# Optimization experiments

Hardware: AMD Instinct MI355X
Metric: run time of the kernel (lower is better)

Reference implementation:

```python
import jax, jax.numpy as jnp
import numpy as np

DIM = 512
CODEBOOK_SIZE = 8192
B, N = 8, 2048
EPS = 1e-12


def setup_inputs() -> dict:
    key = jax.random.key(0)
    k1, k2, k3 = jax.random.split(key, 3)
    x = jax.random.normal(k1, (B, N, DIM), dtype=jnp.float32)
    # matches torch.randn(codebook_size, dim) * dim ** -0.5
    codebook = jax.random.normal(k2, (CODEBOOK_SIZE, DIM), dtype=jnp.float32) * DIM ** -0.5
    # nn.Linear(dim, dim, bias=False) weight, applied as x @ W.T
    W = jax.random.normal(k3, (DIM, DIM), dtype=jnp.float32) * DIM ** -0.5
    return {"x": x, "codebook": codebook, "W": W}


def _l2norm(t):
    return t / jnp.maximum(jnp.linalg.norm(t, axis=-1, keepdims=True), EPS)


def _rotate_from_to(q, x):
    """Rotation trick: forward value == q, gradient flows through x via a
    detached Householder-style rotation (R = I - 2ww^T + 2 q_hat x_hat^T)
    and detached norm rescaling."""
    sg = jax.lax.stop_gradient
    norm_x = jnp.linalg.norm(x, axis=-1, keepdims=True)
    norm_q = jnp.linalg.norm(q, axis=-1, keepdims=True)
    x_hat = x / jnp.maximum(norm_x, EPS)
    q_hat = q / jnp.maximum(norm_q, EPS)
    w = sg(_l2norm(x_hat + q_hat))
    x_hat_d, q_hat_d = sg(x_hat), sg(q_hat)
    e = x
    rotated = (e
               - 2.0 * jnp.sum(e * w, axis=-1, keepdims=True) * w
               + 2.0 * jnp.sum(e * x_hat_d, axis=-1, keepdims=True) * q_hat_d)
    return rotated * sg(norm_q / jnp.maximum(norm_x, EPS))


def reference(x, codebook, W):
    # implicit codebook = Linear(codebook)
    codes = jnp.einsum('cd,ed->ce', codebook, W)  # [C, d]
    d2 = -2.0 * jnp.einsum('bnd,cd->bnc', x, codes) + jnp.sum(codes * codes, axis=-1)
    indices = jnp.argmin(jax.lax.stop_gradient(d2), axis=-1)  # [b, n] int
    quantized = codes[indices]  # gather -> [b, n, d]
    commit_loss = jnp.mean((jax.lax.stop_gradient(x) - quantized) ** 2)
    quantized = _rotate_from_to(quantized, x)
    return quantized, indices, commit_loss
```

## Files before the change

### kernel.cpp

```cpp
#include <hip/hip_runtime.h>


#define DIMK  512
#define CBN   8192
#define MROWS 16384

#define SX 24.0f
#define SC 500.0f
#define INV_SS (1.0f / (SX * SC))
#define DKEY  1231
#define NSLOT 3

#define WS_CODES   0UL
#define WS_XQ      16777216UL
#define WS_CQ      25165824UL
#define WS_NORMS   29360128UL
#define WS_CAND    29392896UL
#define WS_CBH     29392896UL
#define WS_CBL     37781504UL
#define WS_WH      54558720UL
#define WS_WL      55083008UL
#define WS_LOSSP   55607296UL

typedef short s16x8 __attribute__((ext_vector_type(8)));
typedef int   i32x4 __attribute__((ext_vector_type(4)));
typedef float f32x4 __attribute__((ext_vector_type(4)));

__device__ __forceinline__ unsigned short f2bf(float f) {
    unsigned u = __float_as_uint(f);
    unsigned r = u + 0x7FFFu + ((u >> 16) & 1u);
    return (unsigned short)(r >> 16);
}
__device__ __forceinline__ float bf2f(unsigned short h) {
    return __uint_as_float(((unsigned)h) << 16);
}
__device__ __forceinline__ void load_lds16(const void* g, void* l) {
    __builtin_amdgcn_global_load_lds((const __attribute__((address_space(1))) void*)g,
                                     (__attribute__((address_space(3))) void*)l,
                                     16, 0, 0);
}
__device__ __forceinline__ signed char q8(float v, float s) {
    return (signed char)__float2int_rn(fminf(fmaxf(v * s, -127.0f), 127.0f));
}

__global__ __launch_bounds__(256) void prep(
        const float* __restrict__ x, const float* __restrict__ cb, const float* __restrict__ W,
        signed char* __restrict__ xq,
        unsigned short* __restrict__ cbh, unsigned short* __restrict__ cbl,
        unsigned short* __restrict__ wh, unsigned short* __restrict__ wl,
        float* __restrict__ norms) {
    const int b = blockIdx.x;
    const int t = threadIdx.x;
    if (b < 8192) {
        const int i = b * 256 + t;
        float4 v = ((const float4*)x)[i];
        char4 c;
        c.x = q8(v.x, SX); c.y = q8(v.y, SX); c.z = q8(v.z, SX); c.w = q8(v.w, SX);
        ((char4*)xq)[i] = c;
    } else if (b < 12288) {
        const int i = (b - 8192) * 256 + t;
        float4 v = ((const float4*)cb)[i];
        ushort4 h, l;
        h.x = f2bf(v.x); l.x = f2bf(v.x - bf2f(h.x));
        h.y = f2bf(v.y); l.y = f2bf(v.y - bf2f(h.y));
        h.z = f2bf(v.z); l.z = f2bf(v.z - bf2f(h.z));
        h.w = f2bf(v.w); l.w = f2bf(v.w - bf2f(h.w));
        ((ushort4*)cbh)[i] = h;
        ((ushort4*)cbl)[i] = l;
    } else if (b < 12544) {
        const int i = (b - 12288) * 256 + t;
        float4 v = ((const float4*)W)[i];
        ushort4 h, l;
        h.x = f2bf(v.x); l.x = f2bf(v.x - bf2f(h.x));
        h.y = f2bf(v.y); l.y = f2bf(v.y - bf2f(h.y));
        h.z = f2bf(v.z); l.z = f2bf(v.z - bf2f(h.z));
        h.w = f2bf(v.w); l.w = f2bf(v.w - bf2f(h.w));
        ((ushort4*)wh)[i] = h;
        ((ushort4*)wl)[i] = l;
    } else {
        const int i = (b - 12544) * 256 + t;
        norms[i] = 0.0f;
    }
}

__global__ __launch_bounds__(512) void codes_mfma(
        const unsigned short* __restrict__ Ah_g, const unsigned short* __restrict__ Al_g,
        const unsigned short* __restrict__ Bh_g, const unsigned short* __restrict__ Bl_g,
        float* __restrict__ C, signed char* __restrict__ Cq, float* __restrict__ Norms) {
    __shared__ __align__(16) unsigned short Ahi[2][128 * 32];
    __shared__ __align__(16) unsigned short Alo[2][128 * 32];
    __shared__ __align__(16) unsigned short Bhi[2][128 * 32];
    __shared__ __align__(16) unsigned short Blo[2][128 * 32];

    const int t    = threadIdx.x;
    const int w    = t >> 6;
    const int lane = t & 63;
    const int quad = lane >> 4;
    const int l16  = lane & 15;
    const int wm   = w & 3, wn = w >> 2;
    const int rowBase = blockIdx.x * 128;
    const int colBase = blockIdx.y * 128;

    f32x4 acc[2][4];
    #pragma unroll
    for (int i = 0; i < 2; ++i)
        #pragma unroll
        for (int j = 0; j < 4; ++j)
            acc[i][j] = (f32x4)(0.0f);

    const int mr = t >> 2;
    const int kq = ((t & 3) ^ ((t >> 3) & 3)) * 8;
    const size_t gxa = (size_t)(rowBase + mr) * DIMK + kq;
    const size_t gca = (size_t)(colBase + mr) * DIMK + kq;
    const int l0 = w * 512;

    const int swz8 = (quad ^ ((l16 >> 1) & 3)) * 8;

#define CODES_STAGE(NXT, K0)                                   \
    do {                                                       \
        load_lds16(Ah_g + gxa + (K0), &Ahi[NXT][l0]);          \
        load_lds16(Al_g + gxa + (K0), &Alo[NXT][l0]);          \
        load_lds16(Bh_g + gca + (K0), &Bhi[NXT][l0]);          \
        load_lds16(Bl_g + gca + (K0), &Blo[NXT][l0]);          \
    } while (0)

#define CODES_COMPUTE(CUR)                                                                         \
    do {                                                                                           \
        s16x8 ah[2], al[2], bh[4], bl[4];                                                          \
        _Pragma("unroll")                                                                          \
        for (int i = 0; i < 2; ++i) {                                                              \
            const int m = wm * 32 + i * 16 + l16;                                                  \
            ah[i] = *(const s16x8*)&Ahi[CUR][m * 32 + swz8];                                       \
            al[i] = *(const s16x8*)&Alo[CUR][m * 32 + swz8];                                       \
        }                                                                                          \
        _Pragma("unroll")                                                                          \
        for (int j = 0; j < 4; ++j) {                                                              \
            const int n = wn * 64 + j * 16 + l16;                                                  \
            bh[j] = *(const s16x8*)&Bhi[CUR][n * 32 + swz8];                                       \
            bl[j] = *(const s16x8*)&Blo[CUR][n * 32 + swz8];                                       \
        }                                                                                          \
        _Pragma("unroll")                                                                          \
        for (int i = 0; i < 2; ++i)                                                                \
            _Pragma("unroll")                                                                      \
            for (int j = 0; j < 4; ++j) {                                                          \
                acc[i][j] = __builtin_amdgcn_mfma_f32_16x16x32_bf16(ah[i], bh[j], acc[i][j], 0, 0, 0); \
                acc[i][j] = __builtin_amdgcn_mfma_f32_16x16x32_bf16(ah[i], bl[j], acc[i][j], 0, 0, 0); \
                acc[i][j] = __builtin_amdgcn_mfma_f32_16x16x32_bf16(al[i], bh[j], acc[i][j], 0, 0, 0); \
            }                                                                                      \
    } while (0)

    CODES_STAGE(0, 0);
    asm volatile("s_waitcnt vmcnt(0)" ::: "memory");
    __syncthreads();

    for (int k0 = 0; k0 < DIMK; k0 += 64) {
        CODES_STAGE(1, k0 + 32);
        CODES_COMPUTE(0);
        asm volatile("s_waitcnt vmcnt(0)" ::: "memory");
        __syncthreads();
        if (k0 + 64 < DIMK) {
            CODES_STAGE(0, k0 + 64);
            CODES_COMPUTE(1);
            asm volatile("s_waitcnt vmcnt(0)" ::: "memory");
            __syncthreads();
        } else {
            CODES_COMPUTE(1);
        }
    }
#undef CODES_STAGE
#undef CODES_COMPUTE

    #pragma unroll
    for (int i = 0; i < 2; ++i) {
        #pragma unroll
        for (int r = 0; r < 4; ++r) {
            const int row = rowBase + wm * 32 + i * 16 + quad * 4 + r;
            float nsum = 0.0f;
            #pragma unroll
            for (int j = 0; j < 4; ++j) {
                const int col = colBase + wn * 64 + j * 16 + l16;
                const float v = acc[i][j][r];
                C[(size_t)row * DIMK + col] = v;
                Cq[(size_t)row * DIMK + col] = q8(v, SC);
                nsum = fmaf(v, v, nsum);
            }
            nsum += __shfl_xor(nsum, 1, 64);
            nsum += __shfl_xor(nsum, 2, 64);
            nsum += __shfl_xor(nsum, 4, 64);
            nsum += __shfl_xor(nsum, 8, 64);
            if (l16 == 0) atomicAdd(&Norms[row], nsum);
        }
    }
}

__global__ __launch_bounds__(512, 6) void d2_argmin_i8(
        const signed char* __restrict__ Xq,
        const signed char* __restrict__ Cq,
        const float* __restrict__ Norms,
        unsigned* __restrict__ Cand) {
    __shared__ __align__(16) signed char Ash[2][128 * 64];
    __shared__ __align__(16) signed char Bsh[2][128 * 64];

    const int t    = threadIdx.x;
    const int w    = t >> 6;
    const int lane = t & 63;
    const int quad = lane >> 4;
    const int l16  = lane & 15;
    const int wm   = w & 3, wn = w >> 2;
    const int rowBase = blockIdx.x * 128;
    const int colBase = blockIdx.y * 128;

    i32x4 acc[2][4];
    #pragma unroll
    for (int i = 0; i < 2; ++i)
        #pragma unroll
        for (int j = 0; j < 4; ++j)
            acc[i][j] = (i32x4)(0);

    const int mr  = t >> 2;
    const int kcs = ((t & 3) ^ ((t >> 3) & 3)) * 16;
    const size_t gxa = (size_t)(rowBase + mr) * DIMK + kcs;
    const size_t gca = (size_t)(colBase + mr) * DIMK + kcs;
    const int lb = w * 1024;

    const int swz  = (quad ^ ((l16 >> 1) & 3)) * 16;
    const int aoff = (wm * 32 + l16) * 64 + swz;
    const int boff = (wn * 64 + l16) * 64 + swz;

    float nq[4];
    #pragma unroll
    for (int j = 0; j < 4; ++j)
        nq[j] = fmaf(Norms[colBase + wn * 64 + j * 16 + l16], 4096.0f, 65536.0f);

#define D2_STEP(CUR, NXT, K0, DO_STAGE, DO_SYNC)                                                   \
    do {                                                                                           \
        if (DO_STAGE) {                                                                            \
            load_lds16(Xq + gxa + (K0) + 64, &Ash[NXT][lb]);                                       \
            load_lds16(Cq + gca + (K0) + 64, &Bsh[NXT][lb]);                                       \
        }                                                                                          \
        i32x4 af0 = *(const i32x4*)&Ash[CUR][aoff];                                                \
        i32x4 af1 = *(const i32x4*)&Ash[CUR][aoff + 1024];                                         \
        _Pragma("unroll")                                                                          \
        for (int j = 0; j < 4; ++j) {                                                              \
            const i32x4 bfj = *(const i32x4*)&Bsh[CUR][boff + j * 1024];                           \
            acc[0][j] = __builtin_amdgcn_mfma_i32_16x16x64_i8(af0, bfj, acc[0][j], 0, 0, 0);       \
            acc[1][j] = __builtin_amdgcn_mfma_i32_16x16x64_i8(af1, bfj, acc[1][j], 0, 0, 0);       \
        }                                                                                          \
        if (DO_SYNC) {                                                                             \
            asm volatile("s_waitcnt vmcnt(0)" ::: "memory");                                       \
            __syncthreads();                                                                       \
        }                                                                                          \
    } while (0)

    load_lds16(Xq + gxa, &Ash[0][lb]);
    load_lds16(Cq + gca, &Bsh[0][lb]);
    asm volatile("s_waitcnt vmcnt(0)" ::: "memory");
    __syncthreads();

    D2_STEP(0, 1,   0, true,  true);
    D2_STEP(1, 0,  64, true,  true);
    D2_STEP(0, 1, 128, true,  true);
    D2_STEP(1, 0, 192, true,  true);
    D2_STEP(0, 1, 256, true,  true);
    D2_STEP(1, 0, 320, true,  true);
    D2_STEP(0, 1, 384, true,  true);
    D2_STEP(1, 0, 448, false, false);
#undef D2_STEP

    const unsigned colG = colBase + wn * 64 + l16;
    const int subtile = blockIdx.y * 2 + wn;
    const float C2 = -8192.0f * INV_SS;

    #pragma unroll
    for (int i = 0; i < 2; ++i) {
        #pragma unroll
        for (int r = 0; r < 4; ++r) {
            unsigned k[4];
            #pragma unroll
            for (int j = 0; j < 4; ++j) {
                const float kf = fmaf((float)acc[i][j][r], C2, nq[j]);
                int ki = (int)kf;
                ki = ki < 0 ? 0 : ki;
                ki = ki > 524287 ? 524287 : ki;
                k[j] = ((unsigned)ki << 13) | (colG + j * 16);
            }
            unsigned lo01 = min(k[0], k[1]), hi01 = max(k[0], k[1]);
            unsigned lo23 = min(k[2], k[3]), hi23 = max(k[2], k[3]);
            unsigned a0 = min(lo01, lo23);
            unsigned m  = max(lo01, lo23);
            unsigned tt = min(hi01, hi23);
            unsigned a1 = min(m, tt);
            unsigned a2 = max(m, tt);
            #pragma unroll
            for (int mk = 1; mk < 16; mk <<= 1) {
                const unsigned b0 = __shfl_xor(a0, mk, 64);
                const unsigned b1 = __shfl_xor(a1, mk, 64);
                const unsigned b2 = __shfl_xor(a2, mk, 64);
                const unsigned M0 = max(a0, b0);
                const unsigned m1 = min(a1, b1);
                const unsigned n0 = min(a0, b0);
                a2 = min(max(m1, M0), min(a2, b2));
                a1 = min(M0, m1);
                a0 = n0;
            }
            if (l16 == 0) {
                const int row = rowBase + wm * 32 + i * 16 + quad * 4 + r;
                unsigned* slot = Cand + ((size_t)row * 128 + subtile) * NSLOT;
                slot[0] = a0; slot[1] = a1; slot[2] = a2;
            }
        }
    }
}

__global__ __launch_bounds__(256) void refine_gather(
        const float* __restrict__ X, const float* __restrict__ Codes,
        const float* __restrict__ Norms, const unsigned* __restrict__ Cand,
        float* __restrict__ outQ, float* __restrict__ outIdx,
        float* __restrict__ lossP) {
    const int t    = threadIdx.x;
    const int w    = t >> 6;
    const int lane = t & 63;
    const int row  = blockIdx.x * 4 + w;

    const unsigned* cp = Cand + (size_t)row * 128 * NSLOT + lane * 6;
    unsigned sl[6];
    #pragma unroll
    for (int s = 0; s < 6; ++s) sl[s] = cp[s];

    unsigned mn = sl[0];
    #pragma unroll
    for (int s = 1; s < 6; ++s) mn = min(mn, sl[s]);
    #pragma unroll
    for (int mask = 1; mask < 64; mask <<= 1)
        mn = min(mn, (unsigned)__shfl((int)mn, lane ^ mask, 64));
    const unsigned thrp = (((mn >> 13) + DKEY) << 13) | 0x1FFFu;

    const float4 xa = *(const float4*)(X + (size_t)row * DIMK + lane * 8);
    const float4 xb = *(const float4*)(X + (size_t)row * DIMK + lane * 8 + 4);

    float bestD = __builtin_inff();
    unsigned bestIdx = 0xFFFFFFFFu;

    #pragma unroll
    for (int s = 0; s < 6; ++s) {
        unsigned long long bm = __ballot(sl[s] <= thrp);
        while (bm) {
            const int src = __ffsll(bm) - 1;
            bm &= bm - 1;
            const unsigned sv = (unsigned)__shfl((int)sl[s], src, 64);
            const unsigned idx = sv & 0x1FFFu;
            const float4 ca = *(const float4*)(Codes + (size_t)idx * DIMK + lane * 8);
            const float4 cbv = *(const float4*)(Codes + (size_t)idx * DIMK + lane * 8 + 4);
            float s2 = xa.x * ca.x + xa.y * ca.y + xa.z * ca.z + xa.w * ca.w
                     + xb.x * cbv.x + xb.y * cbv.y + xb.z * cbv.z + xb.w * cbv.w;
            #pragma unroll
            for (int mm = 1; mm < 64; mm <<= 1) s2 += __shfl_xor(s2, mm, 64);
            const float d2 = fmaf(-2.0f, s2, Norms[idx]);
            if (d2 < bestD || (d2 == bestD && idx < bestIdx)) { bestD = d2; bestIdx = idx; }
        }
    }

    const float4 qa = *(const float4*)(Codes + (size_t)bestIdx * DIMK + lane * 8);
    const float4 qb = *(const float4*)(Codes + (size_t)bestIdx * DIMK + lane * 8 + 4);
    *(float4*)(outQ + (size_t)row * DIMK + lane * 8) = qa;
    *(float4*)(outQ + (size_t)row * DIMK + lane * 8 + 4) = qb;
    float dx0 = xa.x - qa.x, dx1 = xa.y - qa.y, dx2 = xa.z - qa.z, dx3 = xa.w - qa.w;
    float dy0 = xb.x - qb.x, dy1 = xb.y - qb.y, dy2 = xb.z - qb.z, dy3 = xb.w - qb.w;
    float s = dx0 * dx0 + dx1 * dx1 + dx2 * dx2 + dx3 * dx3
            + dy0 * dy0 + dy1 * dy1 + dy2 * dy2 + dy3 * dy3;
    #pragma unroll
    for (int off = 32; off > 0; off >>= 1) s += __shfl_down(s, off);
    if (lane == 0) {
        lossP[row] = s;
        outIdx[row] = (float)bestIdx;
    }
}

__global__ __launch_bounds__(1024) void finalize_loss(const float* __restrict__ lossPartials,
                                                      float* __restrict__ outLoss) {
    const int t = threadIdx.x;
    const float4* p = (const float4*)lossPartials;
    const float4 a = p[t];
    const float4 b = p[t + 1024];
    const float4 c = p[t + 2048];
    const float4 d = p[t + 3072];
    float s = (a.x + a.y + a.z + a.w) + (b.x + b.y + b.z + b.w)
            + (c.x + c.y + c.z + c.w) + (d.x + d.y + d.z + d.w);
    #pragma unroll
    for (int off = 32; off > 0; off >>= 1) s += __shfl_down(s, off);
    __shared__ float red[16];
    if ((t & 63) == 0) red[t >> 6] = s;
    __syncthreads();
    if (t < 64) {
        float v = (t < 16) ? red[t] : 0.0f;
        v += __shfl_down(v, 8, 64);
        v += __shfl_down(v, 4, 64);
        v += __shfl_down(v, 2, 64);
        v += __shfl_down(v, 1, 64);
        if (t == 0)
            *outLoss = v * (1.0f / (float)((size_t)MROWS * DIMK));
    }
}

extern "C" void kernel_launch(void* const* d_in, const int* in_sizes, int n_in,
                              void* d_out, int out_size, void* d_ws, size_t ws_size,
                              hipStream_t stream) {
    const float* x  = (const float*)d_in[0];
    const float* cb = (const float*)d_in[1];
    const float* W  = (const float*)d_in[2];
    float* out = (float*)d_out;

    char* ws = (char*)d_ws;
    float* codes          = (float*)(ws + WS_CODES);
    signed char* xq       = (signed char*)(ws + WS_XQ);
    signed char* cq       = (signed char*)(ws + WS_CQ);
    float* norms          = (float*)(ws + WS_NORMS);
    unsigned* cand        = (unsigned*)(ws + WS_CAND);
    unsigned short* cbh   = (unsigned short*)(ws + WS_CBH);
    unsigned short* cbl   = (unsigned short*)(ws + WS_CBL);
    unsigned short* wh    = (unsigned short*)(ws + WS_WH);
    unsigned short* wl    = (unsigned short*)(ws + WS_WL);
    float* lossP          = (float*)(ws + WS_LOSSP);

    prep<<<12576, 256, 0, stream>>>(x, cb, W, xq, cbh, cbl, wh, wl, norms);

    codes_mfma<<<dim3(CBN / 128, DIMK / 128), 512, 0, stream>>>(cbh, cbl, wh, wl, codes, cq, norms);

    d2_argmin_i8<<<dim3(MROWS / 128, CBN / 128), 512, 0, stream>>>(xq, cq, norms, cand);

    refine_gather<<<MROWS / 4, 256, 0, stream>>>(x, codes, norms, cand, out,
                                                 out + (size_t)MROWS * DIMK, lossP);
    finalize_loss<<<1, 1024, 0, stream>>>(lossP, out + (size_t)MROWS * DIMK + MROWS);
}
```

Baseline: 265.4 us.

## Halve codes GEMM N-tile, raise MFMA priority, skip refine for single candidate

The codes GEMM tile shrinks from 128x128 to 128x64, doubling the grid to 512 blocks so more CUs are busy. Half the waves now load the B hi part and half the lo part. The int8 distance kernel wraps its MFMA burst in s_setprio to favour the matrix issue over the loads. The refine kernel counts candidates first and, when exactly one survives the threshold, takes it directly and skips the fp32 dot-product rescoring. These are unrelated changes to three kernels, and the smaller GEMM tile lowers data reuse per block.

```diff
diff --git a/kernel.cpp b/kernel.cpp
--- a/kernel.cpp
+++ b/kernel.cpp
@@ -89,8 +89,8 @@
         float* __restrict__ C, signed char* __restrict__ Cq, float* __restrict__ Norms) {
     __shared__ __align__(16) unsigned short Ahi[2][128 * 32];
     __shared__ __align__(16) unsigned short Alo[2][128 * 32];
-    __shared__ __align__(16) unsigned short Bhi[2][128 * 32];
-    __shared__ __align__(16) unsigned short Blo[2][128 * 32];
+    __shared__ __align__(16) unsigned short Bhi[2][64 * 32];
+    __shared__ __align__(16) unsigned short Blo[2][64 * 32];
 
     const int t    = threadIdx.x;
     const int w    = t >> 6;
@@ -99,34 +99,36 @@
     const int l16  = lane & 15;
     const int wm   = w & 3, wn = w >> 2;
     const int rowBase = blockIdx.x * 128;
-    const int colBase = blockIdx.y * 128;
-
-    f32x4 acc[2][4];
+    const int colBase = blockIdx.y * 64;
+
+    f32x4 acc[2][2];
     #pragma unroll
     for (int i = 0; i < 2; ++i)
         #pragma unroll
-        for (int j = 0; j < 4; ++j)
+        for (int j = 0; j < 2; ++j)
             acc[i][j] = (f32x4)(0.0f);
 
-    const int mr = t >> 2;
-    const int kq = ((t & 3) ^ ((t >> 3) & 3)) * 8;
-    const size_t gxa = (size_t)(rowBase + mr) * DIMK + kq;
-    const size_t gca = (size_t)(colBase + mr) * DIMK + kq;
-    const int l0 = w * 512;
+    const int kqA = ((t & 3) ^ ((t >> 3) & 3)) * 8;
+    const size_t gxa = (size_t)(rowBase + (t >> 2)) * DIMK + kqA;
+    const int la = w * 512;
+    const int u   = (w & 3) * 64 + lane;
+    const int kqB = ((u & 3) ^ ((u >> 3) & 3)) * 8;
+    const size_t gcb = (size_t)(colBase + (u >> 2)) * DIMK + kqB;
+    const int lb2 = (w & 3) * 512;
 
     const int swz8 = (quad ^ ((l16 >> 1) & 3)) * 8;
 
-#define CODES_STAGE(NXT, K0)                                   \
-    do {                                                       \
-        load_lds16(Ah_g + gxa + (K0), &Ahi[NXT][l0]);          \
-        load_lds16(Al_g + gxa + (K0), &Alo[NXT][l0]);          \
-        load_lds16(Bh_g + gca + (K0), &Bhi[NXT][l0]);          \
-        load_lds16(Bl_g + gca + (K0), &Blo[NXT][l0]);          \
+#define CODES_STAGE(NXT, K0)                                       \
+    do {                                                           \
+        load_lds16(Ah_g + gxa + (K0), &Ahi[NXT][la]);              \
+        load_lds16(Al_g + gxa + (K0), &Alo[NXT][la]);              \
+        if (w < 4) load_lds16(Bh_g + gcb + (K0), &Bhi[NXT][lb2]);  \
+        else       load_lds16(Bl_g + gcb + (K0), &Blo[NXT][lb2]);  \
     } while (0)
 
 #define CODES_COMPUTE(CUR)                                                                         \
     do {                                                                                           \
-        s16x8 ah[2], al[2], bh[4], bl[4];                                                          \
+        s16x8 ah[2], al[2], bh[2], bl[2];                                                          \
         _Pragma("unroll")                                                                          \
         for (int i = 0; i < 2; ++i) {                                                              \
             const int m = wm * 32 + i * 16 + l16;                                                  \
@@ -134,15 +136,15 @@
             al[i] = *(const s16x8*)&Alo[CUR][m * 32 + swz8];                                       \
         }                                                                                          \
         _Pragma("unroll")                                                                          \
-        for (int j = 0; j < 4; ++j) {                                                              \
-            const int n = wn * 64 + j * 16 + l16;                                                  \
+        for (int j = 0; j < 2; ++j) {                                                              \
+            const int n = wn * 32 + j * 16 + l16;                                                  \
             bh[j] = *(const s16x8*)&Bhi[CUR][n * 32 + swz8];                                       \
             bl[j] = *(const s16x8*)&Blo[CUR][n * 32 + swz8];                                       \
         }                                                                                          \
         _Pragma("unroll")                                                                          \
         for (int i = 0; i < 2; ++i)                                                                \
             _Pragma("unroll")                                                                      \
-            for (int j = 0; j < 4; ++j) {                                                          \
+            for (int j = 0; j < 2; ++j) {                                                          \
                 acc[i][j] = __builtin_amdgcn_mfma_f32_16x16x32_bf16(ah[i], bh[j], acc[i][j], 0, 0, 0); \
                 acc[i][j] = __builtin_amdgcn_mfma_f32_16x16x32_bf16(ah[i], bl[j], acc[i][j], 0, 0, 0); \
                 acc[i][j] = __builtin_amdgcn_mfma_f32_16x16x32_bf16(al[i], bh[j], acc[i][j], 0, 0, 0); \
@@ -177,8 +179,8 @@
             const int row = rowBase + wm * 32 + i * 16 + quad * 4 + r;
             float nsum = 0.0f;
             #pragma unroll
-            for (int j = 0; j < 4; ++j) {
-                const int col = colBase + wn * 64 + j * 16 + l16;
+            for (int j = 0; j < 2; ++j) {
+                const int col = colBase + wn * 32 + j * 16 + l16;
                 const float v = acc[i][j][r];
                 C[(size_t)row * DIMK + col] = v;
                 Cq[(size_t)row * DIMK + col] = q8(v, SC);
@@ -240,12 +242,14 @@
         }                                                                                          \
         i32x4 af0 = *(const i32x4*)&Ash[CUR][aoff];                                                \
         i32x4 af1 = *(const i32x4*)&Ash[CUR][aoff + 1024];                                         \
+        __builtin_amdgcn_s_setprio(1);                                                             \
         _Pragma("unroll")                                                                          \
         for (int j = 0; j < 4; ++j) {                                                              \
             const i32x4 bfj = *(const i32x4*)&Bsh[CUR][boff + j * 1024];                           \
             acc[0][j] = __builtin_amdgcn_mfma_i32_16x16x64_i8(af0, bfj, acc[0][j], 0, 0, 0);       \
             acc[1][j] = __builtin_amdgcn_mfma_i32_16x16x64_i8(af1, bfj, acc[1][j], 0, 0, 0);       \
         }                                                                                          \
+        __builtin_amdgcn_s_setprio(0);                                                             \
         if (DO_SYNC) {                                                                             \
             asm volatile("s_waitcnt vmcnt(0)" ::: "memory");                                       \
             __syncthreads();                                                                       \
@@ -335,28 +339,40 @@
         mn = min(mn, (unsigned)__shfl((int)mn, lane ^ mask, 64));
     const unsigned thrp = (((mn >> 13) + DKEY) << 13) | 0x1FFFu;
 
+    unsigned long long bms[6];
+    int cnt = 0;
+    #pragma unroll
+    for (int s = 0; s < 6; ++s) {
+        bms[s] = __ballot(sl[s] <= thrp);
+        cnt += __popcll(bms[s]);
+    }
+
     const float4 xa = *(const float4*)(X + (size_t)row * DIMK + lane * 8);
     const float4 xb = *(const float4*)(X + (size_t)row * DIMK + lane * 8 + 4);
 
-    float bestD = __builtin_inff();
-    unsigned bestIdx = 0xFFFFFFFFu;
-
-    #pragma unroll
-    for (int s = 0; s < 6; ++s) {
-        unsigned long long bm = __ballot(sl[s] <= thrp);
-        while (bm) {
-            const int src = __ffsll(bm) - 1;
-            bm &= bm - 1;
-            const unsigned sv = (unsigned)__shfl((int)sl[s], src, 64);
-            const unsigned idx = sv & 0x1FFFu;
-            const float4 ca = *(const float4*)(Codes + (size_t)idx * DIMK + lane * 8);
-            const float4 cbv = *(const float4*)(Codes + (size_t)idx * DIMK + lane * 8 + 4);
-            float s2 = xa.x * ca.x + xa.y * ca.y + xa.z * ca.z + xa.w * ca.w
-                     + xb.x * cbv.x + xb.y * cbv.y + xb.z * cbv.z + xb.w * cbv.w;
-            #pragma unroll
-            for (int mm = 1; mm < 64; mm <<= 1) s2 += __shfl_xor(s2, mm, 64);
-            const float d2 = fmaf(-2.0f, s2, Norms[idx]);
-            if (d2 < bestD || (d2 == bestD && idx < bestIdx)) { bestD = d2; bestIdx = idx; }
+    unsigned bestIdx;
+    if (cnt == 1) {
+        bestIdx = mn & 0x1FFFu;
+    } else {
+        float bestD = __builtin_inff();
+        bestIdx = 0xFFFFFFFFu;
+        #pragma unroll
+        for (int s = 0; s < 6; ++s) {
+            unsigned long long bm = bms[s];
+            while (bm) {
+                const int src = __ffsll(bm) - 1;
+                bm &= bm - 1;
+                const unsigned sv = (unsigned)__shfl((int)sl[s], src, 64);
+                const unsigned idx = sv & 0x1FFFu;
+                const float4 ca = *(const float4*)(Codes + (size_t)idx * DIMK + lane * 8);
+                const float4 cbv = *(const float4*)(Codes + (size_t)idx * DIMK + lane * 8 + 4);
+                float s2 = xa.x * ca.x + xa.y * ca.y + xa.z * ca.z + xa.w * ca.w
+                         + xb.x * cbv.x + xb.y * cbv.y + xb.z * cbv.z + xb.w * cbv.w;
+                #pragma unroll
+                for (int mm = 1; mm < 64; mm <<= 1) s2 += __shfl_xor(s2, mm, 64);
+                const float d2 = fmaf(-2.0f, s2, Norms[idx]);
+                if (d2 < bestD || (d2 == bestD && idx < bestIdx)) { bestD = d2; bestIdx = idx; }
+            }
         }
     }
 
@@ -424,7 +440,7 @@
 
     prep<<<12576, 256, 0, stream>>>(x, cb, W, xq, cbh, cbl, wh, wl, norms);
 
-    codes_mfma<<<dim3(CBN / 128, DIMK / 128), 512, 0, stream>>>(cbh, cbl, wh, wl, codes, cq, norms);
+    codes_mfma<<<dim3(CBN / 128, DIMK / 64), 512, 0, stream>>>(cbh, cbl, wh, wl, codes, cq, norms);
 
     d2_argmin_i8<<<dim3(MROWS / 128, CBN / 128), 512, 0, stream>>>(xq, cq, norms, cand);
 
```

New measurement: 271.1 us. 2.1% more time.
